# Optimization experiments

Hardware: AMD Instinct MI355X
Metric: run time of the kernel (lower is better)

The kernel has to match this reference:

```python
import jax, jax.numpy as jnp
import numpy as np

N = 200000
E = 6400000
IN_F = 128
HID = 128
OUT_F = 16
LAYERS = 3
EPS = 1e-5


def setup_inputs() -> dict:
    key = jax.random.key(0)
    ks = jax.random.split(key, 12)
    nodes = jax.random.normal(ks[0], (N, IN_F), dtype=jnp.float32)
    src = jax.random.randint(ks[1], (E,), 0, N, dtype=jnp.int32)
    dst = jax.random.randint(ks[2], (E,), 0, N, dtype=jnp.int32)
    s_in = 1.0 / np.sqrt(IN_F)
    s_h = 1.0 / np.sqrt(HID)
    W_in = jax.random.uniform(ks[3], (IN_F, HID), jnp.float32, -s_in, s_in)
    b_in = jax.random.uniform(ks[4], (HID,), jnp.float32, -s_in, s_in)
    Ws = jax.random.uniform(ks[5], (LAYERS, HID, HID), jnp.float32, -s_h, s_h)
    bs = jax.random.uniform(ks[6], (LAYERS, HID), jnp.float32, -s_h, s_h)
    gammas = jnp.ones((LAYERS, HID), jnp.float32)
    betas = jnp.zeros((LAYERS, HID), jnp.float32)
    W_out = jax.random.uniform(ks[7], (HID, OUT_F), jnp.float32, -s_h, s_h)
    b_out = jax.random.uniform(ks[8], (OUT_F,), jnp.float32, -s_h, s_h)
    return {"nodes": nodes, "src": src, "dst": dst, "W_in": W_in, "b_in": b_in,
            "Ws": Ws, "bs": bs, "gammas": gammas, "betas": betas,
            "W_out": W_out, "b_out": b_out}


def _layernorm(x, g, b):
    mu = jnp.mean(x, axis=-1, keepdims=True)
    var = jnp.var(x, axis=-1, keepdims=True)
    return (x - mu) * jax.lax.rsqrt(var + EPS) * g + b


def reference(nodes, src, dst, W_in, b_in, Ws, bs, gammas, betas, W_out, b_out):
    # in-degree for 'gcn' aggregator normalization: (sum_neigh + self) / (deg + 1)
    deg = jax.ops.segment_sum(jnp.ones((E,), jnp.float32), dst, num_segments=N)
    inv = 1.0 / (deg + 1.0)  # [N]
    x = nodes @ W_in + b_in  # [N, HID]
    for l in range(LAYERS):
        agg = jax.ops.segment_sum(x[src], dst, num_segments=N)  # gather+scatter-add
        h = (agg + x) * inv[:, None]          # gcn mean incl. self
        h = h @ Ws[l] + bs[l]                 # fc_neigh
        h = jax.nn.relu(h)                    # activation (before norm, per DGL)
        x = _layernorm(h, gammas[l], betas[l])
    return x @ W_out + b_out  # [N, OUT_F]
```

## Files before the change

### kernel.cpp

```cpp
#include <hip/hip_runtime.h>

#define N_NODES 200000
#define N_EDGES 6400000
#define HID 128
#define OUTF 16
#define LAYERS 3
#define EPS 1e-5f

#define NRANGES 16
#define RANGE_N 12500
#define NBUCKETS 800
#define BUCKET_N 250
#define BATCH 5000
#define NBATCH (N_EDGES / BATCH)
#define RCAP 405000
#define RBLK (RCAP / BATCH)
#define BCAP 9500

typedef unsigned int u32;

__device__ __forceinline__ unsigned short f2bf(float f){
  unsigned int u = __float_as_uint(f);
  u += 0x7fffu + ((u >> 16) & 1u);
  return (unsigned short)(u >> 16);
}
__device__ __forceinline__ u32 pack2bf(float lo, float hi){
  return (u32)f2bf(lo) | ((u32)f2bf(hi) << 16);
}


__global__ __launch_bounds__(256) void k_initcur(int* __restrict__ range_cursor,
                                                 int* __restrict__ bucket_cursor){
  int t = blockIdx.x * 256 + threadIdx.x;
  if (t < NRANGES) range_cursor[t] = t * RCAP;
  if (t < NBUCKETS) bucket_cursor[t] = t * BCAP;
}


__global__ __launch_bounds__(256) void k_p1(const int* __restrict__ src, const int* __restrict__ dst,
                                            int* __restrict__ range_cursor, u32* __restrict__ ebuf1){
  __shared__ u32 stage[BATCH];
  __shared__ int hist[NRANGES], hist2[NRANGES], hbase[NRANGES], gbase[NRANGES];
  const int tid = threadIdx.x;
  const long e0 = (long)blockIdx.x * BATCH;

  if (tid < NRANGES){ hist[tid] = 0; hist2[tid] = 0; }
  __syncthreads();
  for (int i = tid; i < BATCH; i += 256){
    int d = dst[e0 + i];
    atomicAdd(&hist[d / RANGE_N], 1);
  }
  __syncthreads();
  if (tid == 0){ int run = 0; for (int b = 0; b < NRANGES; b++){ hbase[b] = run; run += hist[b]; } }
  __syncthreads();
  if (tid < NRANGES && hist[tid] > 0) gbase[tid] = atomicAdd(&range_cursor[tid], hist[tid]);
  __syncthreads();
  for (int i = tid; i < BATCH; i += 256){
    int d = dst[e0 + i];
    int s = src[e0 + i];
    int r = d / RANGE_N;
    u32 pk = ((u32)(d - r * RANGE_N) << 18) | (u32)s;
    int p = atomicAdd(&hist2[r], 1);
    stage[hbase[r] + p] = pk;
  }
  __syncthreads();
  for (int b = 0; b < NRANGES; b++){
    int len = hist[b];
    int gb = gbase[b], hb = hbase[b];
    for (int i = tid; i < len; i += 256) ebuf1[gb + i] = stage[hb + i];
  }
}


__global__ __launch_bounds__(256) void k_p2(const u32* __restrict__ ebuf1, const int* __restrict__ range_cursor,
                                            int* __restrict__ bucket_cursor, u32* __restrict__ ebuf2){
  __shared__ u32 stage[BATCH];
  __shared__ int hist[50], hist2[50], hbase[50], gbase[50];
  const int tid = threadIdx.x;
  const int r = blockIdx.x / RBLK;
  const int chunk = blockIdx.x % RBLK;
  const int rlen = range_cursor[r] - r * RCAP;
  const int i0 = chunk * BATCH;
  const int len = min(BATCH, rlen - i0);
  if (len <= 0) return;
  const u32* seg = ebuf1 + (long)r * RCAP + i0;

  if (tid < 50){ hist[tid] = 0; hist2[tid] = 0; }
  __syncthreads();
  for (int i = tid; i < len; i += 256){
    int dl = (int)(seg[i] >> 18);
    atomicAdd(&hist[dl / BUCKET_N], 1);
  }
  __syncthreads();
  if (tid == 0){ int run = 0; for (int b = 0; b < 50; b++){ hbase[b] = run; run += hist[b]; } }
  __syncthreads();
  if (tid < 50 && hist[tid] > 0) gbase[tid] = atomicAdd(&bucket_cursor[r * 50 + tid], hist[tid]);
  __syncthreads();
  for (int i = tid; i < len; i += 256){
    u32 pk = seg[i];
    int b = (int)(pk >> 18) / BUCKET_N;
    int p = atomicAdd(&hist2[b], 1);
    stage[hbase[b] + p] = pk;
  }
  __syncthreads();
  for (int b = 0; b < 50; b++){
    int l = hist[b];
    if (l == 0) continue;
    int gb = gbase[b], hb = hbase[b];
    for (int i = tid; i < l; i += 256) ebuf2[gb + i] = stage[hb + i];
  }
}


__global__ __launch_bounds__(256) void k_scanb(const int* __restrict__ bucket_cursor,
                                               int* __restrict__ bucket_base){
  __shared__ int q[256];
  int tid = threadIdx.x;
  int v[4]; int sum4 = 0;
  if (tid < 200){
    #pragma unroll
    for (int j = 0; j < 4; j++){ int b = 4 * tid + j; v[j] = bucket_cursor[b] - b * BCAP; sum4 += v[j]; }
  }
  q[tid] = sum4; __syncthreads();
  for (int off = 1; off < 256; off <<= 1){
    int t = (tid >= off) ? q[tid - off] : 0;
    __syncthreads();
    q[tid] += t;
    __syncthreads();
  }
  if (tid < 200){
    int run = q[tid] - sum4;
    #pragma unroll
    for (int j = 0; j < 4; j++){ bucket_base[4 * tid + j] = run; run += v[j]; }
  }
}


__global__ __launch_bounds__(256) void k_p3(const u32* __restrict__ ebuf2, const int* __restrict__ bucket_cursor,
                                            const int* __restrict__ bucket_base,
                                            int* __restrict__ csr, int* __restrict__ row_start){
  __shared__ int stage[BCAP];
  __shared__ int hist[BUCKET_N], sbase[BUCKET_N], cur[BUCKET_N];
  __shared__ int q[256];
  const int tid = threadIdx.x;
  const int b = blockIdx.x;
  const int n0 = b * BUCKET_N;
  const int dl0 = (b % 50) * BUCKET_N;
  const int len = min(bucket_cursor[b] - b * BCAP, BCAP);
  const int base = bucket_base[b];
  const u32* seg = ebuf2 + (long)b * BCAP;

  if (tid < BUCKET_N){ hist[tid] = 0; cur[tid] = 0; }
  __syncthreads();
  for (int i = tid; i < len; i += 256){
    int local = (int)(seg[i] >> 18) - dl0;
    local = min(max(local, 0), BUCKET_N - 1);
    atomicAdd(&hist[local], 1);
  }
  __syncthreads();
  {
    int v = (tid < BUCKET_N) ? hist[tid] : 0;
    q[tid] = v; __syncthreads();
    for (int off = 1; off < 256; off <<= 1){
      int t = (tid >= off) ? q[tid - off] : 0;
      __syncthreads();
      q[tid] += t;
      __syncthreads();
    }
    if (tid < BUCKET_N) sbase[tid] = q[tid] - v;
  }
  __syncthreads();
  for (int i = tid; i < len; i += 256){
    u32 pk = seg[i];
    int local = (int)(pk >> 18) - dl0;
    local = min(max(local, 0), BUCKET_N - 1);
    int pos = atomicAdd(&cur[local], 1);
    stage[sbase[local] + pos] = (int)(pk & 0x3FFFFu);
  }
  __syncthreads();
  for (int i = tid; i < len; i += 256) csr[base + i] = stage[i];
  if (tid < BUCKET_N) row_start[n0 + tid] = base + sbase[tid];
  if (b == NBUCKETS - 1 && tid == 0) row_start[N_NODES] = base + len;
}


__global__ __launch_bounds__(256) void k_gemm128(const float* __restrict__ A,
    const float* __restrict__ W, const float* __restrict__ bias,
    const float* __restrict__ gamma, const float* __restrict__ beta,
    float* __restrict__ xout, u32* __restrict__ xbout, int relu_ln)
{
  __shared__ float As[64][132];
  __shared__ float part[64][4][2];
  __shared__ float mu_s[64], rs_s[64];
  __shared__ float gam_s[128], bet_s[128];
  const int tid = threadIdx.x;
  const long row0 = (long)blockIdx.x * 64;

  const float4* A4 = (const float4*)(A + row0 * HID);
  for (int i = tid; i < 64 * 32; i += 256){
    int r = i >> 5, c = i & 31;
    *(float4*)&As[r][c * 4] = A4[r * 32 + c];
  }
  if (relu_ln && tid < 128){ gam_s[tid] = gamma[tid]; bet_s[tid] = beta[tid]; }
  __syncthreads();

  const int cg = tid & 31;
  const int rg = tid >> 5;
  const int c0 = cg * 4;
  float acc[8][4];
  {
    float4 b = *(const float4*)&bias[c0];
    #pragma unroll
    for (int r = 0; r < 8; r++){ acc[r][0]=b.x; acc[r][1]=b.y; acc[r][2]=b.z; acc[r][3]=b.w; }
  }

  for (int k = 0; k < HID; k += 4){
    float4 w0 = *(const float4*)&W[(k + 0) * HID + c0];
    float4 w1 = *(const float4*)&W[(k + 1) * HID + c0];
    float4 w2 = *(const float4*)&W[(k + 2) * HID + c0];
    float4 w3 = *(const float4*)&W[(k + 3) * HID + c0];
    #pragma unroll
    for (int r = 0; r < 8; r++){
      float4 a = *(const float4*)&As[rg * 8 + r][k];
      acc[r][0] = fmaf(a.w, w3.x, fmaf(a.z, w2.x, fmaf(a.y, w1.x, fmaf(a.x, w0.x, acc[r][0]))));
      acc[r][1] = fmaf(a.w, w3.y, fmaf(a.z, w2.y, fmaf(a.y, w1.y, fmaf(a.x, w0.y, acc[r][1]))));
      acc[r][2] = fmaf(a.w, w3.z, fmaf(a.z, w2.z, fmaf(a.y, w1.z, fmaf(a.x, w0.z, acc[r][2]))));
      acc[r][3] = fmaf(a.w, w3.w, fmaf(a.z, w2.w, fmaf(a.y, w1.w, fmaf(a.x, w0.w, acc[r][3]))));
    }
  }

  if (!relu_ln){
    #pragma unroll
    for (int r = 0; r < 8; r++){
      long row = row0 + rg * 8 + r;
      float4 v; v.x = acc[r][0]; v.y = acc[r][1]; v.z = acc[r][2]; v.w = acc[r][3];
      *(float4*)&xout[row * HID + c0] = v;
      uint2 p; p.x = pack2bf(v.x, v.y); p.y = pack2bf(v.z, v.w);
      *(uint2*)&xbout[(row * HID + c0) >> 1] = p;
    }
  } else {
    __syncthreads();
    #pragma unroll
    for (int r = 0; r < 8; r++){
      float4 v;
      v.x = fmaxf(acc[r][0], 0.f); v.y = fmaxf(acc[r][1], 0.f);
      v.z = fmaxf(acc[r][2], 0.f); v.w = fmaxf(acc[r][3], 0.f);
      *(float4*)&As[rg * 8 + r][c0] = v;
    }
    __syncthreads();
    {
      int row = tid >> 2, qq = tid & 3;
      float s = 0.f, s2 = 0.f;
      #pragma unroll 8
      for (int c = 0; c < 32; c++){ float v = As[row][qq * 32 + c]; s += v; s2 += v * v; }
      part[row][qq][0] = s; part[row][qq][1] = s2;
    }
    __syncthreads();
    if (tid < 64){
      float s  = part[tid][0][0] + part[tid][1][0] + part[tid][2][0] + part[tid][3][0];
      float s2 = part[tid][0][1] + part[tid][1][1] + part[tid][2][1] + part[tid][3][1];
      float mu = s * (1.f / HID);
      float var = s2 * (1.f / HID) - mu * mu;
      mu_s[tid] = mu;
      rs_s[tid] = 1.f / sqrtf(var + EPS);
    }
    __syncthreads();
    for (int i = tid; i < 64 * 32; i += 256){
      int r = i >> 5, c4 = (i & 31) * 4;
      float4 v = *(float4*)&As[r][c4];
      float mu = mu_s[r], rs = rs_s[r];
      v.x = (v.x - mu) * rs * gam_s[c4 + 0] + bet_s[c4 + 0];
      v.y = (v.y - mu) * rs * gam_s[c4 + 1] + bet_s[c4 + 1];
      v.z = (v.z - mu) * rs * gam_s[c4 + 2] + bet_s[c4 + 2];
      v.w = (v.w - mu) * rs * gam_s[c4 + 3] + bet_s[c4 + 3];
      long row = row0 + r;
      *(float4*)&xout[row * HID + c4] = v;
      uint2 p; p.x = pack2bf(v.x, v.y); p.y = pack2bf(v.z, v.w);
      *(uint2*)&xbout[(row * HID + c4) >> 1] = p;
    }
  }
}


__global__ __launch_bounds__(256) void k_agg(const int* __restrict__ row_start, const int* __restrict__ csr,
    const uint2* __restrict__ xb2, const float* __restrict__ x, float* __restrict__ h)
{
  int gid  = blockIdx.x * 256 + threadIdx.x;
  int node = gid >> 6;
  int lane = gid & 63;
  int half = lane >> 5, col = lane & 31;
  int s0 = row_start[node], s1 = row_start[node + 1];
  float a0 = 0.f, a1 = 0.f, a2 = 0.f, a3 = 0.f;

  if (s0 < s1){
    const int s1m1 = s1 - 1;
    for (int base = s0; base < s1; base += 16){
      int idx[8];
      #pragma unroll
      for (int j = 0; j < 8; j++) idx[j] = csr[min(base + 2*j + half, s1m1)];
      uint2 p[8];
      #pragma unroll
      for (int j = 0; j < 8; j++) p[j] = xb2[(long)idx[j] * 32 + col];
      #pragma unroll
      for (int j = 0; j < 8; j++){
        bool act = (base + 2*j + half) < s1;
        float v0 = __uint_as_float(p[j].x << 16);
        float v1 = __uint_as_float(p[j].x & 0xffff0000u);
        float v2 = __uint_as_float(p[j].y << 16);
        float v3 = __uint_as_float(p[j].y & 0xffff0000u);
        a0 += act ? v0 : 0.f;
        a1 += act ? v1 : 0.f;
        a2 += act ? v2 : 0.f;
        a3 += act ? v3 : 0.f;
      }
    }
  }

  a0 += __shfl_down(a0, 32);
  a1 += __shfl_down(a1, 32);
  a2 += __shfl_down(a2, 32);
  a3 += __shfl_down(a3, 32);

  if (half == 0){
    float inv = 1.f / (float)(s1 - s0 + 1);
    long bidx = (long)node * HID + col * 4;
    float4 xs = *(const float4*)&x[bidx];
    float4 r;
    r.x = (a0 + xs.x) * inv;
    r.y = (a1 + xs.y) * inv;
    r.z = (a2 + xs.z) * inv;
    r.w = (a3 + xs.w) * inv;
    *(float4*)&h[bidx] = r;
  }
}


__global__ __launch_bounds__(256) void k_gemm_out(const float* __restrict__ x,
    const float* __restrict__ Wo, const float* __restrict__ bo, float* __restrict__ out)
{
  __shared__ float As[16][132];
  __shared__ float Wl[HID * OUTF];
  const int tid = threadIdx.x;
  const long row0 = (long)blockIdx.x * 16;
  const float4* A4 = (const float4*)(x + row0 * HID);
  for (int i = tid; i < 16 * 32; i += 256){
    int r = i >> 5, c = i & 31;
    *(float4*)&As[r][c * 4] = A4[r * 32 + c];
  }
  for (int i = tid; i < HID * OUTF; i += 256) Wl[i] = Wo[i];
  __syncthreads();
  int col = tid & 15, r = tid >> 4;
  float acc = bo[col];
  for (int k = 0; k < HID; k += 4){
    float4 a = *(const float4*)&As[r][k];
    acc = fmaf(a.x, Wl[(k + 0) * OUTF + col],
          fmaf(a.y, Wl[(k + 1) * OUTF + col],
          fmaf(a.z, Wl[(k + 2) * OUTF + col],
          fmaf(a.w, Wl[(k + 3) * OUTF + col], acc))));
  }
  out[(row0 + r) * OUTF + col] = acc;
}


extern "C" void kernel_launch(void* const* d_in, const int* in_sizes, int n_in,
                              void* d_out, int out_size, void* d_ws, size_t ws_size,
                              hipStream_t stream)
{
  (void)in_sizes; (void)n_in; (void)out_size; (void)ws_size;
  const float* nodes = (const float*)d_in[0];
  const int*   src   = (const int*)d_in[1];
  const int*   dst   = (const int*)d_in[2];
  const float* W_in  = (const float*)d_in[3];
  const float* b_in  = (const float*)d_in[4];
  const float* Ws    = (const float*)d_in[5];
  const float* bs    = (const float*)d_in[6];
  const float* gam   = (const float*)d_in[7];
  const float* bet   = (const float*)d_in[8];
  const float* W_out = (const float*)d_in[9];
  const float* b_out = (const float*)d_in[10];
  float* out = (float*)d_out;

  size_t off = 0;
  auto bump = [&](size_t bytes) -> char* {
    char* p = (char*)d_ws + off;
    off = (off + bytes + 255) & ~(size_t)255;
    return p;
  };
  int* row_start     = (int*)bump((N_NODES + 1) * sizeof(int));
  int* range_cursor  = (int*)bump(NRANGES * sizeof(int));
  int* bucket_cursor = (int*)bump(NBUCKETS * sizeof(int));
  int* bucket_base   = (int*)bump((NBUCKETS + 1) * sizeof(int));
  int* csr           = (int*)bump((size_t)N_EDGES * sizeof(int));
  float* x           = (float*)bump((size_t)N_NODES * HID * sizeof(float));
  float* h           = (float*)bump((size_t)N_NODES * HID * sizeof(float));
  u32* xb            = (u32*)bump((size_t)N_NODES * HID * sizeof(unsigned short));

  u32* ebuf1 = (u32*)x;
  u32* ebuf2 = (u32*)h;

  k_initcur<<<4, 256, 0, stream>>>(range_cursor, bucket_cursor);
  k_p1<<<NBATCH, 256, 0, stream>>>(src, dst, range_cursor, ebuf1);
  k_p2<<<NRANGES * RBLK, 256, 0, stream>>>(ebuf1, range_cursor, bucket_cursor, ebuf2);
  k_scanb<<<1, 256, 0, stream>>>(bucket_cursor, bucket_base);
  k_p3<<<NBUCKETS, 256, 0, stream>>>(ebuf2, bucket_cursor, bucket_base, csr, row_start);

  k_gemm128<<<N_NODES / 64, 256, 0, stream>>>(nodes, W_in, b_in, nullptr, nullptr, x, xb, 0);
  for (int l = 0; l < LAYERS; l++){
    k_agg<<<N_NODES / 4, 256, 0, stream>>>(row_start, csr, (const uint2*)xb, x, h);
    k_gemm128<<<N_NODES / 64, 256, 0, stream>>>(h, Ws + (size_t)l * HID * HID, bs + l * HID,
                                                gam + l * HID, bet + l * HID, x, xb, 1);
  }
  k_gemm_out<<<N_NODES / 16, 256, 0, stream>>>(x, W_out, b_out, out);
}
```

Before: 1.444 ms.

## Widen aggregation gathers to 16-byte loads with four edges per wavefront step

The gather-aggregate kernel now has each lane load a uint4 (8 bf16 features), so a 64-lane wavefront processes four neighbor rows at once instead of two. It adds an unmasked main loop over 32 edges that prefetches the next batch of CSR indices, followed by 16-edge and masked remainder tails, then a two-level shuffle reduction. The self-feature load is hoisted ahead of the loop. The aim is fewer, wider memory transactions and less per-edge masking overhead, at the cost of more registers and tail code.

```diff
diff --git a/kernel.cpp b/kernel.cpp
--- a/kernel.cpp
+++ b/kernel.cpp
@@ -283,54 +283,122 @@
 
 
 __global__ __launch_bounds__(256) void k_agg(const int* __restrict__ row_start, const int* __restrict__ csr,
-    const uint2* __restrict__ xb2, const float* __restrict__ x, float* __restrict__ h)
+    const uint4* __restrict__ xb4, const float* __restrict__ x, float* __restrict__ h)
 {
   int gid  = blockIdx.x * 256 + threadIdx.x;
   int node = gid >> 6;
   int lane = gid & 63;
-  int half = lane >> 5, col = lane & 31;
+  int q = lane >> 4;
+  int c = lane & 15;
   int s0 = row_start[node], s1 = row_start[node + 1];
-  float a0 = 0.f, a1 = 0.f, a2 = 0.f, a3 = 0.f;
-
-  if (s0 < s1){
+  const uint4* xbc = xb4 + c;
+
+  float4 xsa = {0.f,0.f,0.f,0.f}, xsb = {0.f,0.f,0.f,0.f};
+  if (q == 0){
+    xsa = *(const float4*)&x[(long)node * HID + c * 8];
+    xsb = *(const float4*)&x[(long)node * HID + c * 8 + 4];
+  }
+
+  float a[8] = {0.f,0.f,0.f,0.f,0.f,0.f,0.f,0.f};
+
+  int base = s0;
+  int idx[8];
+  if (base + 32 <= s1){
+    #pragma unroll
+    for (int j = 0; j < 8; j++) idx[j] = csr[base + 4*j + q];
+  }
+  while (base + 32 <= s1){
+    uint4 p[8];
+    #pragma unroll
+    for (int j = 0; j < 8; j++) p[j] = xbc[(long)idx[j] * 16];
+    base += 32;
+    if (base + 32 <= s1){
+      #pragma unroll
+      for (int j = 0; j < 8; j++) idx[j] = csr[base + 4*j + q];
+    }
+    #pragma unroll
+    for (int j = 0; j < 8; j++){
+      a[0] += __uint_as_float(p[j].x << 16);
+      a[1] += __uint_as_float(p[j].x & 0xffff0000u);
+      a[2] += __uint_as_float(p[j].y << 16);
+      a[3] += __uint_as_float(p[j].y & 0xffff0000u);
+      a[4] += __uint_as_float(p[j].z << 16);
+      a[5] += __uint_as_float(p[j].z & 0xffff0000u);
+      a[6] += __uint_as_float(p[j].w << 16);
+      a[7] += __uint_as_float(p[j].w & 0xffff0000u);
+    }
+  }
+  if (base + 16 <= s1){
+    int ti[4];
+    #pragma unroll
+    for (int j = 0; j < 4; j++) ti[j] = csr[base + 4*j + q];
+    uint4 p[4];
+    #pragma unroll
+    for (int j = 0; j < 4; j++) p[j] = xbc[(long)ti[j] * 16];
+    #pragma unroll
+    for (int j = 0; j < 4; j++){
+      a[0] += __uint_as_float(p[j].x << 16);
+      a[1] += __uint_as_float(p[j].x & 0xffff0000u);
+      a[2] += __uint_as_float(p[j].y << 16);
+      a[3] += __uint_as_float(p[j].y & 0xffff0000u);
+      a[4] += __uint_as_float(p[j].z << 16);
+      a[5] += __uint_as_float(p[j].z & 0xffff0000u);
+      a[6] += __uint_as_float(p[j].w << 16);
+      a[7] += __uint_as_float(p[j].w & 0xffff0000u);
+    }
+    base += 16;
+  }
+  if (base < s1){
     const int s1m1 = s1 - 1;
-    for (int base = s0; base < s1; base += 16){
-      int idx[8];
-      #pragma unroll
-      for (int j = 0; j < 8; j++) idx[j] = csr[min(base + 2*j + half, s1m1)];
-      uint2 p[8];
-      #pragma unroll
-      for (int j = 0; j < 8; j++) p[j] = xb2[(long)idx[j] * 32 + col];
-      #pragma unroll
-      for (int j = 0; j < 8; j++){
-        bool act = (base + 2*j + half) < s1;
-        float v0 = __uint_as_float(p[j].x << 16);
-        float v1 = __uint_as_float(p[j].x & 0xffff0000u);
-        float v2 = __uint_as_float(p[j].y << 16);
-        float v3 = __uint_as_float(p[j].y & 0xffff0000u);
-        a0 += act ? v0 : 0.f;
-        a1 += act ? v1 : 0.f;
-        a2 += act ? v2 : 0.f;
-        a3 += act ? v3 : 0.f;
-      }
-    }
-  }
-
-  a0 += __shfl_down(a0, 32);
-  a1 += __shfl_down(a1, 32);
-  a2 += __shfl_down(a2, 32);
-  a3 += __shfl_down(a3, 32);
-
-  if (half == 0){
+    const int rem = s1 - base;
+    int ti[4];
+    #pragma unroll
+    for (int j = 0; j < 4; j++) ti[j] = csr[min(base + 4*j + q, s1m1)];
+    uint4 p[4];
+    #pragma unroll
+    for (int j = 0; j < 4; j++) p[j] = xbc[(long)ti[j] * 16];
+    #pragma unroll
+    for (int j = 0; j < 4; j++){
+      bool act = (4*j + q) < rem;
+      float f0 = __uint_as_float(p[j].x << 16);
+      float f1 = __uint_as_float(p[j].x & 0xffff0000u);
+      float f2 = __uint_as_float(p[j].y << 16);
+      float f3 = __uint_as_float(p[j].y & 0xffff0000u);
+      float f4 = __uint_as_float(p[j].z << 16);
+      float f5 = __uint_as_float(p[j].z & 0xffff0000u);
+      float f6 = __uint_as_float(p[j].w << 16);
+      float f7 = __uint_as_float(p[j].w & 0xffff0000u);
+      a[0] += act ? f0 : 0.f;
+      a[1] += act ? f1 : 0.f;
+      a[2] += act ? f2 : 0.f;
+      a[3] += act ? f3 : 0.f;
+      a[4] += act ? f4 : 0.f;
+      a[5] += act ? f5 : 0.f;
+      a[6] += act ? f6 : 0.f;
+      a[7] += act ? f7 : 0.f;
+    }
+  }
+
+  #pragma unroll
+  for (int k = 0; k < 8; k++){
+    a[k] += __shfl_down(a[k], 32);
+    a[k] += __shfl_down(a[k], 16);
+  }
+
+  if (q == 0){
     float inv = 1.f / (float)(s1 - s0 + 1);
-    long bidx = (long)node * HID + col * 4;
-    float4 xs = *(const float4*)&x[bidx];
-    float4 r;
-    r.x = (a0 + xs.x) * inv;
-    r.y = (a1 + xs.y) * inv;
-    r.z = (a2 + xs.z) * inv;
-    r.w = (a3 + xs.w) * inv;
-    *(float4*)&h[bidx] = r;
+    long bidx = (long)node * HID + c * 8;
+    float4 r0, r1;
+    r0.x = (a[0] + xsa.x) * inv;
+    r0.y = (a[1] + xsa.y) * inv;
+    r0.z = (a[2] + xsa.z) * inv;
+    r0.w = (a[3] + xsa.w) * inv;
+    r1.x = (a[4] + xsb.x) * inv;
+    r1.y = (a[5] + xsb.y) * inv;
+    r1.z = (a[6] + xsb.z) * inv;
+    r1.w = (a[7] + xsb.w) * inv;
+    *(float4*)&h[bidx] = r0;
+    *(float4*)&h[bidx + 4] = r1;
   }
 }
 
@@ -406,7 +474,7 @@
 
   k_gemm128<<<N_NODES / 64, 256, 0, stream>>>(nodes, W_in, b_in, nullptr, nullptr, x, xb, 0);
   for (int l = 0; l < LAYERS; l++){
-    k_agg<<<N_NODES / 4, 256, 0, stream>>>(row_start, csr, (const uint2*)xb, x, h);
+    k_agg<<<N_NODES / 4, 256, 0, stream>>>(row_start, csr, (const uint4*)xb, x, h);
     k_gemm128<<<N_NODES / 64, 256, 0, stream>>>(h, Ws + (size_t)l * HID * HID, bs + l * HID,
                                                 gam + l * HID, bet + l * HID, x, xb, 1);
   }
```

Result: no change. 1.457 ms (+0.8%).
